# Performance work log

Measured on AMD Instinct MI355X. Metric: run time of the kernel, lower is better.

## Reference

```python
import jax, jax.numpy as jnp
import numpy as np
from jax import lax

EPS = 1e-6
C = 192
SHAPE = (2, C, 32, 48, 48)


def setup_inputs() -> dict:
    key = jax.random.key(0)
    ks = jax.random.split(key, 20)
    d = {
        "xs": jax.random.normal(ks[0], SHAPE, jnp.float32),
        "xt": jax.random.normal(ks[1], SHAPE, jnp.float32),
        "ln_w": jnp.ones((C,), jnp.float32),
        "ln_b": jnp.zeros((C,), jnp.float32),
        "qk_sp_w": jax.random.normal(ks[2], (C,), jnp.float32) * 0.1,
        "qk_sp_b": jax.random.normal(ks[3], (C,), jnp.float32) * 0.1,
        "v_sp_w": jax.random.normal(ks[4], (C,), jnp.float32) * 0.1,
        "v_sp_b": jax.random.normal(ks[5], (C,), jnp.float32) * 0.1,
        "qk_tm_w": jax.random.normal(ks[6], (C,), jnp.float32) * 0.1,
        "qk_tm_b": jax.random.normal(ks[7], (C,), jnp.float32) * 0.1,
        "v_tm_w": jax.random.normal(ks[8], (C,), jnp.float32) * 0.1,
        "v_tm_b": jax.random.normal(ks[9], (C,), jnp.float32) * 0.1,
        "attn_w": jax.random.normal(ks[10], (C, 1, 4, 4, 4), jnp.float32) * 0.1,
        "attn_b": jax.random.normal(ks[11], (C,), jnp.float32) * 0.1,
        "grn_gamma": jax.random.normal(ks[12], (1, C, 1, 1, 1), jnp.float32) * 0.1,
        "grn_beta": jax.random.normal(ks[13], (1, C, 1, 1, 1), jnp.float32) * 0.1,
        "proj_w": jax.random.normal(ks[14], (C,), jnp.float32) * 0.1,
        "proj_b": jax.random.normal(ks[15], (C,), jnp.float32) * 0.1,
    }
    return d


def _cvec(v):  # [C] -> broadcastable over [B,C,D,H,W]
    return v[None, :, None, None, None]


def _dw1(x, w, b):  # depthwise 1x1x1 conv == per-channel affine
    return x * _cvec(w) + _cvec(b)


def _ln_cf(x, w, b):  # channels-first LayerNorm over channel dim
    mean = jnp.mean(x, axis=1, keepdims=True)
    var = jnp.mean((x - mean) ** 2, axis=1, keepdims=True)
    y = (x - mean) * lax.rsqrt(var + EPS)
    return _cvec(w) * y + _cvec(b)


def _grn(x, gamma, beta):
    gx = jnp.sqrt(jnp.sum(x * x, axis=(2, 3, 4), keepdims=True))  # [B,C,1,1,1]
    nx = gx / (jnp.mean(gx, axis=1, keepdims=True) + EPS)
    return gamma * (x * nx) + beta + x


def reference(xs, xt, ln_w, ln_b, qk_sp_w, qk_sp_b, v_sp_w, v_sp_b,
              qk_tm_w, qk_tm_b, v_tm_w, v_tm_b, attn_w, attn_b,
              grn_gamma, grn_beta, proj_w, proj_b):
    x0 = xs
    xsn = _ln_cf(xs, ln_w, ln_b)
    qk = _dw1(xsn, qk_sp_w, qk_sp_b) + _dw1(xt, qk_tm_w, qk_tm_b)
    v = _dw1(xsn, v_sp_w, v_sp_b) + _dw1(xt, v_tm_w, v_tm_b)
    a = jax.nn.silu(qk)
    # depthwise 4x4x4 conv, padding 3, dilation 2 (spatial-size preserving)
    a = lax.conv_general_dilated(
        a, attn_w, window_strides=(1, 1, 1), padding=[(3, 3)] * 3,
        rhs_dilation=(2, 2, 2),
        dimension_numbers=("NCDHW", "OIDHW", "NCDHW"),
        feature_group_count=a.shape[1]) + _cvec(attn_b)
    x = a * v
    x = _grn(x, grn_gamma, grn_beta)
    x = _dw1(x, proj_w, proj_b)  # proj conv; DropPath(0) is identity
    return x0 + x
```

## Files before the change

### kernel.cpp

```cpp
#include <hip/hip_runtime.h>
#include <math.h>

#define BB 2
#define CC 192
#define DD 32
#define HH 48
#define WW 48
#define HWs (HH*WW)
#define SS (DD*HH*WW)
#define BS (BB*SS)
#define NTOT (BB*CC*SS)
#define EPSV 1e-6f

typedef unsigned short ushort;

__device__ __forceinline__ ushort pack_bf16(float x) {
    unsigned u = __float_as_uint(x);
    u += 0x7FFFu + ((u >> 16) & 1u);
    return (ushort)(u >> 16);
}
__device__ __forceinline__ float bf16_lo(unsigned u) { return __uint_as_float(u << 16); }
__device__ __forceinline__ float bf16_hi(unsigned u) { return __uint_as_float(u & 0xFFFF0000u); }

#define CG 48
__global__ __launch_bounds__(256) void k1_ln_av(
    const float* __restrict__ xs, const float* __restrict__ xt,
    const float* __restrict__ ln_w, const float* __restrict__ ln_b,
    const float* __restrict__ qk_sp_w, const float* __restrict__ qk_sp_b,
    const float* __restrict__ v_sp_w, const float* __restrict__ v_sp_b,
    const float* __restrict__ qk_tm_w, const float* __restrict__ qk_tm_b,
    const float* __restrict__ v_tm_w, const float* __restrict__ v_tm_b,
    ushort* __restrict__ a_out, ushort* __restrict__ v_out)
{
    __shared__ float w_all[10][CC];
    __shared__ float sred[2][4][64];
    int tid = threadIdx.x;
    if (tid < CC) {
        w_all[0][tid] = ln_w[tid];   w_all[1][tid] = ln_b[tid];
        w_all[2][tid] = qk_sp_w[tid]; w_all[3][tid] = qk_sp_b[tid];
        w_all[4][tid] = qk_tm_w[tid]; w_all[5][tid] = qk_tm_b[tid];
        w_all[6][tid] = v_sp_w[tid];  w_all[7][tid] = v_sp_b[tid];
        w_all[8][tid] = v_tm_w[tid];  w_all[9][tid] = v_tm_b[tid];
    }
    __syncthreads();

    int tx = tid & 63, wy = tid >> 6;
    int p0 = blockIdx.x * 64;
    int b = p0 / SS;
    int s = (p0 % SS) + tx;

    const float* xsp = xs + ((size_t)(b * CC + wy * CG)) * SS + s;
    float xv[CG];
    float sum = 0.f, ssum = 0.f;
    #pragma unroll
    for (int i = 0; i < CG; ++i) {
        float v = xsp[(size_t)i * SS];
        xv[i] = v; sum += v; ssum += v * v;
    }
    sred[0][wy][tx] = sum;
    sred[1][wy][tx] = ssum;
    __syncthreads();
    sum  = sred[0][0][tx] + sred[0][1][tx] + sred[0][2][tx] + sred[0][3][tx];
    ssum = sred[1][0][tx] + sred[1][1][tx] + sred[1][2][tx] + sred[1][3][tx];
    float mean = sum * (1.0f / CC);
    float var  = ssum * (1.0f / CC) - mean * mean;
    float rstd = rsqrtf(var + EPSV);

    const float* xtp = xt + ((size_t)(b * CC + wy * CG)) * SS + s;
    ushort* ap = a_out + ((size_t)(b * CC + wy * CG)) * SS + s;
    ushort* vp = v_out + ((size_t)(b * CC + wy * CG)) * SS + s;
    #pragma unroll
    for (int i = 0; i < CG; ++i) {
        int c = wy * CG + i;
        float t  = xtp[(size_t)i * SS];
        float xn = (xv[i] - mean) * rstd * w_all[0][c] + w_all[1][c];
        float qk = xn * w_all[2][c] + w_all[3][c] + t * w_all[4][c] + w_all[5][c];
        float vv = xn * w_all[6][c] + w_all[7][c] + t * w_all[8][c] + w_all[9][c];
        float av = qk / (1.f + __expf(-qk));
        ap[(size_t)i * SS] = pack_bf16(av);
        vp[(size_t)i * SS] = pack_bf16(vv);
    }
}

#define ODT 4
#define OHT 24
#define NP 10
#define NR 30
#define RSD 28
#define PSD (NR*RSD)
#define TILE_DW (NP*PSD)

__global__ __launch_bounds__(576, 5) void k2_conv(
    const ushort* __restrict__ a_in, const ushort* __restrict__ v_in,
    const float* __restrict__ attn_w, const float* __restrict__ attn_b,
    ushort* __restrict__ x_out, float* __restrict__ ssq)
{
    __shared__ unsigned tile[TILE_DW];
    __shared__ float wts[64];
    int tid = threadIdx.x;
    int blk = blockIdx.x;
    int bc = blk >> 4;
    int rem = blk & 15;
    int d0 = (rem >> 1) * ODT;
    int h0 = (rem & 1) * OHT;
    int c = bc % CC;

    const ushort* abase = a_in + (size_t)bc * SS;
    for (int i = tid; i < TILE_DW; i += 576) {
        int p = i / PSD;
        int r2 = i - p * PSD;
        int r = r2 / RSD;
        int q2 = r2 - r * RSD;
        int id = d0 - 3 + p;
        int ih = h0 - 3 + r;
        int iw = q2 * 2 - 4;
        unsigned val = 0;
        if ((unsigned)id < (unsigned)DD && (unsigned)ih < (unsigned)HH &&
            (unsigned)iw < 47u)
            val = *(const unsigned*)(abase + (size_t)id * HWs + ih * WW + iw);
        tile[i] = val;
    }
    if (tid < 64) wts[tid] = attn_w[c * 64 + tid];
    __syncthreads();
    float bias = attn_b[c];

    int strip = tid % 6;
    int ohl = (tid / 6) % 24;
    int odl = tid / 144;
    int ow0 = strip * 8;

    float acc[8];
    #pragma unroll
    for (int j = 0; j < 8; ++j) acc[j] = 0.f;

    #pragma unroll
    for (int kd = 0; kd < 4; ++kd) {
        int p = odl + 2 * kd;
        #pragma unroll
        for (int kh = 0; kh < 4; ++kh) {
            int r = ohl + 2 * kh;
            int bd = p * PSD + r * RSD + strip * 4;
            unsigned u[8];
            *(uint4*)&u[0] = *(const uint4*)&tile[bd];
            *(uint4*)&u[4] = *(const uint4*)&tile[bd + 4];
            float wf[16];
            #pragma unroll
            for (int m = 0; m < 8; ++m) {
                wf[2*m]   = bf16_lo(u[m]);
                wf[2*m+1] = bf16_hi(u[m]);
            }
            float4 wv = *(const float4*)&wts[(kd * 4 + kh) * 4];
            #pragma unroll
            for (int j = 0; j < 8; ++j) {
                float a0 = fmaf(wf[j + 1], wv.x, acc[j]);
                float a1 = fmaf(wf[j + 3], wv.y, a0);
                float a2 = fmaf(wf[j + 5], wv.z, a1);
                acc[j]   = fmaf(wf[j + 7], wv.w, a2);
            }
        }
    }

    int od = d0 + odl, oh = h0 + ohl;
    size_t g = (size_t)bc * SS + (size_t)od * HWs + oh * WW + ow0;
    unsigned uv[4];
    *(uint4*)&uv[0] = *(const uint4*)(v_in + g);
    float ssql = 0.f;
    ushort pk[8];
    #pragma unroll
    for (int m = 0; m < 4; ++m) {
        float v0 = bf16_lo(uv[m]);
        float v1 = bf16_hi(uv[m]);
        float x0 = (acc[2*m]     + bias) * v0;
        float x1 = (acc[2*m + 1] + bias) * v1;
        ssql += x0 * x0 + x1 * x1;
        pk[2*m]     = pack_bf16(x0);
        pk[2*m + 1] = pack_bf16(x1);
    }
    *(uint4*)&x_out[g] = *(uint4*)&pk[0];

    #pragma unroll
    for (int off = 32; off > 0; off >>= 1)
        ssql += __shfl_down(ssql, off);
    if ((tid & 63) == 0) atomicAdd(&ssq[bc], ssql);
}

__global__ __launch_bounds__(384) void k3_scale(
    const float* __restrict__ ssq,
    const float* __restrict__ grn_gamma, const float* __restrict__ grn_beta,
    const float* __restrict__ proj_w, const float* __restrict__ proj_b,
    float* __restrict__ AB)
{
    __shared__ float gxs[BB*CC];
    __shared__ float msum[BB];
    int tid = threadIdx.x;
    float gx = sqrtf(ssq[tid]);
    gxs[tid] = gx;
    __syncthreads();
    if (tid < BB) {
        float s = 0.f;
        for (int c2 = 0; c2 < CC; ++c2) s += gxs[tid * CC + c2];
        msum[tid] = s * (1.0f / CC);
    }
    __syncthreads();
    int b = tid / CC, c2 = tid % CC;
    float nx = gx / (msum[b] + EPSV);
    float A  = proj_w[c2] * (1.f + grn_gamma[c2] * nx);
    float B2 = proj_w[c2] * grn_beta[c2] + proj_b[c2];
    AB[tid] = A;
    AB[BB*CC + tid] = B2;
}

__global__ __launch_bounds__(256) void k4_final(
    const float* __restrict__ xs, const ushort* __restrict__ xv,
    const float* __restrict__ AB, float* __restrict__ out)
{
    int i = blockIdx.x * 256 + threadIdx.x;
    size_t g = (size_t)i * 8;
    int bc = (int)(g / SS);
    float A  = AB[bc];
    float B2 = AB[BB*CC + bc];
    uint4 xr = *(const uint4*)&xv[g];
    unsigned hx[4];
    *(uint4*)hx = xr;
    float4 s0 = *(const float4*)&xs[g];
    float4 s1 = *(const float4*)&xs[g + 4];
    float o[8];
    float sv[8] = {s0.x, s0.y, s0.z, s0.w, s1.x, s1.y, s1.z, s1.w};
    #pragma unroll
    for (int m = 0; m < 4; ++m) {
        o[2*m]   = fmaf(A, bf16_lo(hx[m]), sv[2*m])   + B2;
        o[2*m+1] = fmaf(A, bf16_hi(hx[m]), sv[2*m+1]) + B2;
    }
    *(float4*)&out[g]     = ((float4*)o)[0];
    *(float4*)&out[g + 4] = ((float4*)o)[1];
}

extern "C" void kernel_launch(void* const* d_in, const int* in_sizes, int n_in,
                              void* d_out, int out_size, void* d_ws, size_t ws_size,
                              hipStream_t stream) {
    const float* xs      = (const float*)d_in[0];
    const float* xt      = (const float*)d_in[1];
    const float* ln_w    = (const float*)d_in[2];
    const float* ln_b    = (const float*)d_in[3];
    const float* qk_sp_w = (const float*)d_in[4];
    const float* qk_sp_b = (const float*)d_in[5];
    const float* v_sp_w  = (const float*)d_in[6];
    const float* v_sp_b  = (const float*)d_in[7];
    const float* qk_tm_w = (const float*)d_in[8];
    const float* qk_tm_b = (const float*)d_in[9];
    const float* v_tm_w  = (const float*)d_in[10];
    const float* v_tm_b  = (const float*)d_in[11];
    const float* attn_w  = (const float*)d_in[12];
    const float* attn_b  = (const float*)d_in[13];
    const float* grn_g   = (const float*)d_in[14];
    const float* grn_b   = (const float*)d_in[15];
    const float* proj_w  = (const float*)d_in[16];
    const float* proj_b  = (const float*)d_in[17];
    float* out = (float*)d_out;

    ushort* a_buf = (ushort*)d_ws;
    ushort* v_buf = a_buf + (size_t)NTOT;
    ushort* x_buf = v_buf + (size_t)NTOT;
    float* ssq    = (float*)(x_buf + (size_t)NTOT);
    float* AB     = ssq + BB*CC;

    hipMemsetAsync(ssq, 0, BB*CC*sizeof(float), stream);

    k1_ln_av<<<BS/64, 256, 0, stream>>>(xs, xt, ln_w, ln_b,
        qk_sp_w, qk_sp_b, v_sp_w, v_sp_b,
        qk_tm_w, qk_tm_b, v_tm_w, v_tm_b, a_buf, v_buf);

    k2_conv<<<BB*CC*16, 576, 0, stream>>>(a_buf, v_buf,
        attn_w, attn_b, x_buf, ssq);

    k3_scale<<<1, 384, 0, stream>>>(ssq, grn_g, grn_b, proj_w, proj_b, AB);

    k4_final<<<NTOT/8/256, 256, 0, stream>>>(xs, x_buf, AB, out);
}
```

Before: 812.4 us.

## Restructure LN kernel to per-thread pixel pairs; vectorize conv tile loads

The LayerNorm/gating kernel changes shape. Each thread now handles two adjacent pixels across all 192 channels, using float2 loads and packed bf16x2 stores. This removes the shared-memory cross-wave channel reduction, but xs is now read twice and the grid shrinks to 288 blocks. The conv kernel's halo tile load now reads four bf16 values per 64-bit load, with the bounds check adjusted to match. The conv kernel's launch-bounds minimum-blocks hint is relaxed from 5 to 2, which frees registers at possible cost to occupancy.

New measurement: 708.8 us. 12.8% less time.

```diff
diff --git a/kernel.cpp b/kernel.cpp
--- a/kernel.cpp
+++ b/kernel.cpp
@@ -19,10 +19,12 @@
     u += 0x7FFFu + ((u >> 16) & 1u);
     return (ushort)(u >> 16);
 }
+__device__ __forceinline__ unsigned pack_bf16x2(float lo, float hi) {
+    return (unsigned)pack_bf16(lo) | ((unsigned)pack_bf16(hi) << 16);
+}
 __device__ __forceinline__ float bf16_lo(unsigned u) { return __uint_as_float(u << 16); }
 __device__ __forceinline__ float bf16_hi(unsigned u) { return __uint_as_float(u & 0xFFFF0000u); }
 
-#define CG 48
 __global__ __launch_bounds__(256) void k1_ln_av(
     const float* __restrict__ xs, const float* __restrict__ xt,
     const float* __restrict__ ln_w, const float* __restrict__ ln_b,
@@ -33,10 +35,9 @@
     ushort* __restrict__ a_out, ushort* __restrict__ v_out)
 {
     __shared__ float w_all[10][CC];
-    __shared__ float sred[2][4][64];
     int tid = threadIdx.x;
     if (tid < CC) {
-        w_all[0][tid] = ln_w[tid];   w_all[1][tid] = ln_b[tid];
+        w_all[0][tid] = ln_w[tid];    w_all[1][tid] = ln_b[tid];
         w_all[2][tid] = qk_sp_w[tid]; w_all[3][tid] = qk_sp_b[tid];
         w_all[4][tid] = qk_tm_w[tid]; w_all[5][tid] = qk_tm_b[tid];
         w_all[6][tid] = v_sp_w[tid];  w_all[7][tid] = v_sp_b[tid];
@@ -44,41 +45,40 @@
     }
     __syncthreads();
 
-    int tx = tid & 63, wy = tid >> 6;
-    int p0 = blockIdx.x * 64;
+    int p0 = blockIdx.x * 512;
     int b = p0 / SS;
-    int s = (p0 % SS) + tx;
-
-    const float* xsp = xs + ((size_t)(b * CC + wy * CG)) * SS + s;
-    float xv[CG];
-    float sum = 0.f, ssum = 0.f;
-    #pragma unroll
-    for (int i = 0; i < CG; ++i) {
-        float v = xsp[(size_t)i * SS];
-        xv[i] = v; sum += v; ssum += v * v;
-    }
-    sred[0][wy][tx] = sum;
-    sred[1][wy][tx] = ssum;
-    __syncthreads();
-    sum  = sred[0][0][tx] + sred[0][1][tx] + sred[0][2][tx] + sred[0][3][tx];
-    ssum = sred[1][0][tx] + sred[1][1][tx] + sred[1][2][tx] + sred[1][3][tx];
-    float mean = sum * (1.0f / CC);
-    float var  = ssum * (1.0f / CC) - mean * mean;
-    float rstd = rsqrtf(var + EPSV);
-
-    const float* xtp = xt + ((size_t)(b * CC + wy * CG)) * SS + s;
-    ushort* ap = a_out + ((size_t)(b * CC + wy * CG)) * SS + s;
-    ushort* vp = v_out + ((size_t)(b * CC + wy * CG)) * SS + s;
-    #pragma unroll
-    for (int i = 0; i < CG; ++i) {
-        int c = wy * CG + i;
-        float t  = xtp[(size_t)i * SS];
-        float xn = (xv[i] - mean) * rstd * w_all[0][c] + w_all[1][c];
-        float qk = xn * w_all[2][c] + w_all[3][c] + t * w_all[4][c] + w_all[5][c];
-        float vv = xn * w_all[6][c] + w_all[7][c] + t * w_all[8][c] + w_all[9][c];
-        float av = qk / (1.f + __expf(-qk));
-        ap[(size_t)i * SS] = pack_bf16(av);
-        vp[(size_t)i * SS] = pack_bf16(vv);
+    int s = (p0 % SS) + tid * 2;
+
+    const float* xsp = xs + (size_t)b * CC * SS + s;
+    const float* xtp = xt + (size_t)b * CC * SS + s;
+
+    float sum0 = 0.f, sum1 = 0.f, ssum0 = 0.f, ssum1 = 0.f;
+    #pragma unroll 4
+    for (int c = 0; c < CC; ++c) {
+        float2 v = *(const float2*)(xsp + (size_t)c * SS);
+        sum0 += v.x; ssum0 += v.x * v.x;
+        sum1 += v.y; ssum1 += v.y * v.y;
+    }
+    float mean0 = sum0 * (1.0f / CC), mean1 = sum1 * (1.0f / CC);
+    float rstd0 = rsqrtf(ssum0 * (1.0f / CC) - mean0 * mean0 + EPSV);
+    float rstd1 = rsqrtf(ssum1 * (1.0f / CC) - mean1 * mean1 + EPSV);
+
+    ushort* ap = a_out + (size_t)b * CC * SS + s;
+    ushort* vp = v_out + (size_t)b * CC * SS + s;
+    #pragma unroll 4
+    for (int c = 0; c < CC; ++c) {
+        float2 v = *(const float2*)(xsp + (size_t)c * SS);
+        float2 t = *(const float2*)(xtp + (size_t)c * SS);
+        float xn0 = (v.x - mean0) * rstd0 * w_all[0][c] + w_all[1][c];
+        float xn1 = (v.y - mean1) * rstd1 * w_all[0][c] + w_all[1][c];
+        float qk0 = xn0 * w_all[2][c] + w_all[3][c] + t.x * w_all[4][c] + w_all[5][c];
+        float qk1 = xn1 * w_all[2][c] + w_all[3][c] + t.y * w_all[4][c] + w_all[5][c];
+        float vv0 = xn0 * w_all[6][c] + w_all[7][c] + t.x * w_all[8][c] + w_all[9][c];
+        float vv1 = xn1 * w_all[6][c] + w_all[7][c] + t.y * w_all[8][c] + w_all[9][c];
+        float a0 = qk0 / (1.f + __expf(-qk0));
+        float a1 = qk1 / (1.f + __expf(-qk1));
+        *(unsigned*)(ap + (size_t)c * SS) = pack_bf16x2(a0, a1);
+        *(unsigned*)(vp + (size_t)c * SS) = pack_bf16x2(vv0, vv1);
     }
 }
 
@@ -90,7 +90,7 @@
 #define PSD (NR*RSD)
 #define TILE_DW (NP*PSD)
 
-__global__ __launch_bounds__(576, 5) void k2_conv(
+__global__ __launch_bounds__(576, 2) void k2_conv(
     const ushort* __restrict__ a_in, const ushort* __restrict__ v_in,
     const float* __restrict__ attn_w, const float* __restrict__ attn_b,
     ushort* __restrict__ x_out, float* __restrict__ ssq)
@@ -106,7 +106,8 @@
     int c = bc % CC;
 
     const ushort* abase = a_in + (size_t)bc * SS;
-    for (int i = tid; i < TILE_DW; i += 576) {
+    for (int i2 = tid; i2 < TILE_DW / 2; i2 += 576) {
+        int i = i2 * 2;
         int p = i / PSD;
         int r2 = i - p * PSD;
         int r = r2 / RSD;
@@ -114,11 +115,11 @@
         int id = d0 - 3 + p;
         int ih = h0 - 3 + r;
         int iw = q2 * 2 - 4;
-        unsigned val = 0;
+        uint2 val = make_uint2(0u, 0u);
         if ((unsigned)id < (unsigned)DD && (unsigned)ih < (unsigned)HH &&
-            (unsigned)iw < 47u)
-            val = *(const unsigned*)(abase + (size_t)id * HWs + ih * WW + iw);
-        tile[i] = val;
+            (unsigned)iw < 45u)
+            val = *(const uint2*)(abase + (size_t)id * HWs + ih * WW + iw);
+        *(uint2*)&tile[i] = val;
     }
     if (tid < 64) wts[tid] = attn_w[c * 64 + tid];
     __syncthreads();
@@ -266,7 +267,7 @@
 
     hipMemsetAsync(ssq, 0, BB*CC*sizeof(float), stream);
 
-    k1_ln_av<<<BS/64, 256, 0, stream>>>(xs, xt, ln_w, ln_b,
+    k1_ln_av<<<BS/512, 256, 0, stream>>>(xs, xt, ln_w, ln_b,
         qk_sp_w, qk_sp_b, v_sp_w, v_sp_b,
         qk_tm_w, qk_tm_b, v_tm_w, v_tm_b, a_buf, v_buf);
 
```
